# Kernel optimization log

Hardware: AMD Instinct MI355X
Metric: run time of the kernel (lower is better)

## Reference

```python
import jax, jax.numpy as jnp
import numpy as np
import math

B, S, HID, H = 2, 1024, 512, 8
D = HID // H  # 64
EPS = 1e-24


def setup_inputs() -> dict:
    key = jax.random.key(0)
    ks = jax.random.split(key, 12)
    s = 0.02
    return {
        "input_tensor": jax.random.normal(ks[0], (B, S, HID), dtype=jnp.float32),
        "attention_mask": jnp.zeros((B, 1, S, S), dtype=jnp.float32),
        # Linear weights stored as [in, out] (y = x @ W + b)
        "Wq": jax.random.normal(ks[1], (HID, HID), dtype=jnp.float32) * s,
        "bq": jnp.zeros((HID,), dtype=jnp.float32),
        "Wk": jax.random.normal(ks[2], (HID, HID), dtype=jnp.float32) * s,
        "bk": jnp.zeros((HID,), dtype=jnp.float32),
        "Wv": jax.random.normal(ks[3], (HID, HID), dtype=jnp.float32) * s,
        "bv": jnp.zeros((HID,), dtype=jnp.float32),
        # order_affine: Linear(2*D, 1)
        "order_w": jax.random.normal(ks[4], (2 * D,), dtype=jnp.float32) * s,
        "order_b": jnp.zeros((), dtype=jnp.float32),
        # distance_affine: Linear(2*D, 1)
        "dist_w": jax.random.normal(ks[5], (2 * D,), dtype=jnp.float32) * s,
        "dist_b": jnp.zeros((), dtype=jnp.float32),
        "scalar": jax.random.normal(ks[6], (1,), dtype=jnp.float32),
    }


def _heads(x):  # [B,S,HID] -> [B,H,S,D]
    return x.reshape(B, S, H, D).transpose(0, 2, 1, 3)


def reference(input_tensor, attention_mask, Wq, bq, Wk, bk, Wv, bv,
              order_w, order_b, dist_w, dist_b, scalar):
    scale = math.sqrt(D)

    mixed_q = input_tensor @ Wq + bq            # [B,S,HID]
    mixed_k = input_tensor @ Wk + bk
    mixed_v = input_tensor @ Wv + bv

    qh = _heads(mixed_q)                        # [B,H,S,D]
    kh = _heads(mixed_k)
    vh = _heads(mixed_v)

    scores = jnp.einsum('bhid,bhjd->bhij', qh, kh)   # [B,H,S,S]
    origin_scores = scores

    # --- order bias: sigmoid(affine(cat(q_i, k_j))) decomposed (same math,
    # avoids materializing the [B,H,S,S,2D] concat the torch code builds) ---
    q_ord = jnp.einsum('bhid,d->bhi', qh, order_w[:D])    # [B,H,S]
    k_ord = jnp.einsum('bhjd,d->bhj', kh, order_w[D:])
    pr_order = jax.nn.sigmoid(q_ord[..., :, None] + k_ord[..., None, :] + order_b)
    gd_order = jnp.triu(jnp.ones((S, S), dtype=scores.dtype), k=1)  # 1 where j>i
    error_order = (jnp.log(pr_order + EPS) * gd_order
                   + jnp.log(1.0 - pr_order + EPS) * (1.0 - gd_order))

    # --- distance bias ---
    idx = jnp.arange(S)
    gd_distance = jnp.log(jnp.abs(idx[None, :] - idx[:, None]).astype(scores.dtype) + 1.0)
    q_dst = jnp.einsum('bhid,d->bhi', qh, dist_w[:D])
    k_dst = jnp.einsum('bhjd,d->bhj', kh, dist_w[D:])
    pr_distance = q_dst[..., :, None] + k_dst[..., None, :] + dist_b   # [B,H,S,S]
    error_distance = -jnp.square(gd_distance - pr_distance) * jnp.square(scalar[0]) * 0.5

    adj_scores = scores + error_order + error_distance

    def _probs(sc):
        return jax.nn.softmax(sc / scale + attention_mask, axis=-1)

    attention_probs = _probs(adj_scores)
    origin_attention_probs = _probs(origin_scores)

    return (mixed_q, mixed_k, vh, attention_probs, origin_attention_probs)
```

## Files before the change

kernel.cpp:

```cpp
#include <hip/hip_runtime.h>
#include <math.h>

#define Sdim 1024
#define HIDdim 512
#define Hnum 8
#define Ddim 64

typedef __attribute__((ext_vector_type(4))) float f32x4;
typedef __attribute__((ext_vector_type(8))) short short8;
typedef __attribute__((ext_vector_type(4))) unsigned short ushort4v;

static __device__ __forceinline__ unsigned short f2bf(float x) {
    union { float f; unsigned u; } v; v.f = x;
    unsigned r = v.u + 0x7fffu + ((v.u >> 16) & 1u);
    return (unsigned short)(r >> 16);
}

__global__ __launch_bounds__(256) void qkv_gemm(
    const float* __restrict__ X,
    const float* __restrict__ Wq, const float* __restrict__ bq,
    const float* __restrict__ Wk, const float* __restrict__ bk,
    const float* __restrict__ Wv, const float* __restrict__ bv,
    float* __restrict__ outq, float* __restrict__ outk, float* __restrict__ outv)
{
    __shared__ unsigned short Ws[64][72];
    __shared__ unsigned short Xs[64][72];

    const int mb = blockIdx.x;
    const int nb = blockIdx.y;
    const int which = nb >> 3;
    const int n0 = (nb & 7) * 64;
    const float* __restrict__ W    = (which == 0) ? Wq : (which == 1) ? Wk : Wv;
    const float* __restrict__ bias = (which == 0) ? bq : (which == 1) ? bk : bv;

    const int t    = threadIdx.x;
    const int lane = t & 63;
    const int w    = t >> 6;
    const int g    = lane >> 4;
    const int c    = lane & 15;
    const int m0r  = mb * 64;

    f32x4 acc[4];
#pragma unroll
    for (int f = 0; f < 4; ++f) { f32x4 z = {0.f, 0.f, 0.f, 0.f}; acc[f] = z; }

    for (int kt = 0; kt < 512; kt += 64) {
        __syncthreads();
        {
            const int row = t >> 2, kb = (t & 3) * 16;
            const float* __restrict__ src = &X[(size_t)(m0r + row) * HIDdim + kt + kb];
#pragma unroll
            for (int i = 0; i < 4; ++i) {
                const f32x4 v = *(const f32x4*)&src[4 * i];
                ushort4v p;
                p.x = f2bf(v.x); p.y = f2bf(v.y); p.z = f2bf(v.z); p.w = f2bf(v.w);
                *(ushort4v*)&Xs[row][kb + 4 * i] = p;
            }
        }
#pragma unroll
        for (int p = 0; p < 4; ++p) {
            const int kr   = p * 16 + (t >> 4);
            const int nloc = (t & 15) * 4;
            const f32x4 v = *(const f32x4*)&W[(size_t)(kt + kr) * HIDdim + n0 + nloc];
            Ws[nloc + 0][kr] = f2bf(v.x);
            Ws[nloc + 1][kr] = f2bf(v.y);
            Ws[nloc + 2][kr] = f2bf(v.z);
            Ws[nloc + 3][kr] = f2bf(v.w);
        }
        __syncthreads();
        const short8 a0 = *(const short8*)&Ws[w * 16 + c][g * 8];
        const short8 a1 = *(const short8*)&Ws[w * 16 + c][32 + g * 8];
#pragma unroll
        for (int f = 0; f < 4; ++f) {
            const short8 b0 = *(const short8*)&Xs[f * 16 + c][g * 8];
            const short8 b1 = *(const short8*)&Xs[f * 16 + c][32 + g * 8];
            acc[f] = __builtin_amdgcn_mfma_f32_16x16x32_bf16(a0, b0, acc[f], 0, 0, 0);
            acc[f] = __builtin_amdgcn_mfma_f32_16x16x32_bf16(a1, b1, acc[f], 0, 0, 0);
        }
    }

    const int nql = w * 16 + g * 4;
    const f32x4 bb = *(const f32x4*)&bias[n0 + nql];
#pragma unroll
    for (int f = 0; f < 4; ++f) {
        const int m = m0r + f * 16 + c;
        f32x4 v = acc[f] + bb;
        if (which == 2) {
            const int b = m >> 10, s = m & 1023;
            const int h = nb & 7;
            *(f32x4*)&outv[((((size_t)b * Hnum + h) * Sdim) + s) * Ddim + nql] = v;
        } else {
            float* __restrict__ o = (which == 0) ? outq : outk;
            *(f32x4*)&o[(size_t)m * HIDdim + n0 + nql] = v;
        }
    }
}

__global__ __launch_bounds__(512, 4) void attn_kernel(
    const float* __restrict__ mq, const float* __restrict__ mk,
    const float* __restrict__ mask,
    const float* __restrict__ order_w, const float* __restrict__ order_b_p,
    const float* __restrict__ dist_w,  const float* __restrict__ dist_b_p,
    const float* __restrict__ scalar_p,
    float* __restrict__ out_adj, float* __restrict__ out_orig)
{
    __shared__ unsigned short Qs[16][72];
    __shared__ unsigned short Ks[128][72];
    __shared__ float ko_s[Sdim];
    __shared__ float kd_s[Sdim];
    __shared__ float gdl[Sdim];
    __shared__ float qo_s[16], qd_s[16];
    __shared__ float red_s[16][8];

    const int t    = threadIdx.x;
    const int lane = t & 63;
    const int w    = t >> 6;
    const int g    = lane >> 4;
    const int c    = lane & 15;

    const int blk = blockIdx.x;
    const int ib  = blk & 63;
    const int bh  = blk >> 6;
    const int b   = bh >> 3;
    const int h   = bh & 7;
    const int i0  = ib * 16;
    const int i   = i0 + c;

    const float order_b = order_b_p[0];
    const float dist_b  = dist_b_p[0];
    const float sc      = scalar_p[0];
    const float sc2h    = 0.5f * sc * sc;
    const float mscale  = 0.125f;

    const int row8 = t >> 3;
    const int dc8  = (t & 7) * 8;
    const f32x4 owk0 = *(const f32x4*)&order_w[Ddim + dc8];
    const f32x4 owk1 = *(const f32x4*)&order_w[Ddim + dc8 + 4];
    const f32x4 dwk0 = *(const f32x4*)&dist_w[Ddim + dc8];
    const f32x4 dwk1 = *(const f32x4*)&dist_w[Ddim + dc8 + 4];

    if (t < 256) {
        const int drow = t >> 4, dcol = (t & 15) * 4;
        const f32x4 owq = *(const f32x4*)&order_w[dcol];
        const f32x4 dwq = *(const f32x4*)&dist_w[dcol];
        const f32x4 v = *(const f32x4*)&mq[((size_t)b * Sdim + i0 + drow) * HIDdim + h * Ddim + dcol];
        float po = v.x * owq.x + v.y * owq.y + v.z * owq.z + v.w * owq.w;
        float pd = v.x * dwq.x + v.y * dwq.y + v.z * dwq.z + v.w * dwq.w;
#pragma unroll
        for (int o = 1; o < 16; o <<= 1) { po += __shfl_xor(po, o); pd += __shfl_xor(pd, o); }
        if ((t & 15) == 0) { qo_s[drow] = po; qd_s[drow] = pd; }
        ushort4v p;
        p.x = f2bf(v.x); p.y = f2bf(v.y); p.z = f2bf(v.z); p.w = f2bf(v.w);
        *(ushort4v*)&Qs[drow][dcol] = p;
    }
    {
        const int idx = t * 2;
        gdl[idx]     = __logf((float)idx + 1.0f);
        gdl[idx + 1] = __logf((float)idx + 2.0f);
    }
    __syncthreads();

    const short8 qf0 = *(const short8*)&Qs[c][g * 8];
    const short8 qf1 = *(const short8*)&Qs[c][32 + g * 8];

    f32x4 acc[8];
#pragma unroll
    for (int it = 0; it < 8; ++it) { f32x4 z = {0.f, 0.f, 0.f, 0.f}; acc[it] = z; }

#pragma unroll
    for (int it = 0; it < 8; ++it) {
        __syncthreads();
        const int kt0 = it * 128;
#pragma unroll
        for (int sub = 0; sub < 2; ++sub) {
            const int row = sub * 64 + row8;
            const float* __restrict__ src =
                &mk[((size_t)b * Sdim + kt0 + row) * HIDdim + h * Ddim + dc8];
            const f32x4 v0 = *(const f32x4*)&src[0];
            const f32x4 v1 = *(const f32x4*)&src[4];
            float po = v0.x * owk0.x + v0.y * owk0.y + v0.z * owk0.z + v0.w * owk0.w
                     + v1.x * owk1.x + v1.y * owk1.y + v1.z * owk1.z + v1.w * owk1.w;
            float pd = v0.x * dwk0.x + v0.y * dwk0.y + v0.z * dwk0.z + v0.w * dwk0.w
                     + v1.x * dwk1.x + v1.y * dwk1.y + v1.z * dwk1.z + v1.w * dwk1.w;
#pragma unroll
            for (int o = 1; o < 8; o <<= 1) { po += __shfl_xor(po, o); pd += __shfl_xor(pd, o); }
            if ((t & 7) == 0) { ko_s[kt0 + row] = po; kd_s[kt0 + row] = pd; }
            ushort4v p0, p1;
            p0.x = f2bf(v0.x); p0.y = f2bf(v0.y); p0.z = f2bf(v0.z); p0.w = f2bf(v0.w);
            p1.x = f2bf(v1.x); p1.y = f2bf(v1.y); p1.z = f2bf(v1.z); p1.w = f2bf(v1.w);
            *(ushort4v*)&Ks[row][dc8]     = p0;
            *(ushort4v*)&Ks[row][dc8 + 4] = p1;
        }
        __syncthreads();
        const short8 kf0 = *(const short8*)&Ks[w * 16 + c][g * 8];
        const short8 kf1 = *(const short8*)&Ks[w * 16 + c][32 + g * 8];
        acc[it] = __builtin_amdgcn_mfma_f32_16x16x32_bf16(kf0, qf0, acc[it], 0, 0, 0);
        acc[it] = __builtin_amdgcn_mfma_f32_16x16x32_bf16(kf1, qf1, acc[it], 0, 0, 0);
    }

    const size_t obase = (size_t)bh * Sdim * Sdim;
    const float* __restrict__ mrow = &mask[((size_t)b * Sdim + i) * Sdim];

    float s0 = 0.0f;
#pragma unroll
    for (int it = 0; it < 8; ++it) {
        const int j0 = it * 128 + w * 16 + g * 4;
        const f32x4 mk4 = *(const f32x4*)&mrow[j0];
        f32x4 l = acc[it] * mscale + mk4;
        acc[it] = l;
        s0 += __expf(l[0]) + __expf(l[1]) + __expf(l[2]) + __expf(l[3]);
    }
    s0 += __shfl_xor(s0, 16);
    s0 += __shfl_xor(s0, 32);
    if (lane < 16) red_s[lane][w] = s0;
    __syncthreads();
    f32x4 ra = *(const f32x4*)&red_s[c][0];
    f32x4 rb = *(const f32x4*)&red_s[c][4];
    const float inv0 = __builtin_amdgcn_rcpf(ra[0] + ra[1] + ra[2] + ra[3]
                                           + rb[0] + rb[1] + rb[2] + rb[3]);
    {
        float* __restrict__ orow = out_orig + obase + (size_t)i * Sdim;
#pragma unroll
        for (int it = 0; it < 8; ++it) {
            const int j0 = it * 128 + w * 16 + g * 4;
            const f32x4 l = acc[it];
            f32x4 p;
            p[0] = __expf(l[0]) * inv0; p[1] = __expf(l[1]) * inv0;
            p[2] = __expf(l[2]) * inv0; p[3] = __expf(l[3]) * inv0;
            *(f32x4*)&orow[j0] = p;
        }
    }

    const float qo = qo_s[c] + order_b;
    const float qd = qd_s[c] + dist_b;
    float s1 = 0.0f;
#pragma unroll
    for (int it = 0; it < 8; ++it) {
        const int j0 = it * 128 + w * 16 + g * 4;
        const f32x4 ko4 = *(const f32x4*)&ko_s[j0];
        const f32x4 kd4 = *(const f32x4*)&kd_s[j0];
        f32x4 l = acc[it];
#pragma unroll
        for (int r = 0; r < 4; ++r) {
            const int j = j0 + r;
            const float z    = qo + ko4[r];
            const float targ = (j > i) ? -z : z;
            const float pe   = -__logf(1.0f + __expf(targ));
            const int   dl   = (i > j) ? (i - j) : (j - i);
            const float df   = gdl[dl] - (qd + kd4[r]);
            l[r] += (pe - sc2h * df * df) * mscale;
            s1 += __expf(l[r]);
        }
        acc[it] = l;
    }
    __syncthreads();
    s1 += __shfl_xor(s1, 16);
    s1 += __shfl_xor(s1, 32);
    if (lane < 16) red_s[lane][w] = s1;
    __syncthreads();
    ra = *(const f32x4*)&red_s[c][0];
    rb = *(const f32x4*)&red_s[c][4];
    const float inv1 = __builtin_amdgcn_rcpf(ra[0] + ra[1] + ra[2] + ra[3]
                                           + rb[0] + rb[1] + rb[2] + rb[3]);
    {
        float* __restrict__ arow = out_adj + obase + (size_t)i * Sdim;
#pragma unroll
        for (int it = 0; it < 8; ++it) {
            const int j0 = it * 128 + w * 16 + g * 4;
            const f32x4 l = acc[it];
            f32x4 p;
            p[0] = __expf(l[0]) * inv1; p[1] = __expf(l[1]) * inv1;
            p[2] = __expf(l[2]) * inv1; p[3] = __expf(l[3]) * inv1;
            *(f32x4*)&arow[j0] = p;
        }
    }
}

extern "C" void kernel_launch(void* const* d_in, const int* in_sizes, int n_in,
                              void* d_out, int out_size, void* d_ws, size_t ws_size,
                              hipStream_t stream) {
    const float* X    = (const float*)d_in[0];
    const float* mask = (const float*)d_in[1];
    const float* Wq   = (const float*)d_in[2];
    const float* bq   = (const float*)d_in[3];
    const float* Wk   = (const float*)d_in[4];
    const float* bk   = (const float*)d_in[5];
    const float* Wv   = (const float*)d_in[6];
    const float* bv   = (const float*)d_in[7];
    const float* ow   = (const float*)d_in[8];
    const float* ob   = (const float*)d_in[9];
    const float* dw   = (const float*)d_in[10];
    const float* db   = (const float*)d_in[11];
    const float* sc   = (const float*)d_in[12];

    float* out     = (float*)d_out;
    float* outq    = out;
    float* outk    = out + 1048576;
    float* outv    = out + 2097152;
    float* outadj  = out + 3145728;
    float* outorig = out + 19922944;

    qkv_gemm<<<dim3(32, 24), 256, 0, stream>>>(X, Wq, bq, Wk, bk, Wv, bv,
                                               outq, outk, outv);
    attn_kernel<<<dim3(1024), 512, 0, stream>>>(outq, outk, mask,
                                                ow, ob, dw, db, sc,
                                                outadj, outorig);
}
```

Measured before the change: 82.28 us.

## Precompute bf16 Q/K and bias projections in a separate prep kernel

```diff
diff --git a/kernel.cpp b/kernel.cpp
--- a/kernel.cpp
+++ b/kernel.cpp
@@ -96,20 +96,73 @@
     }
 }
 
+__global__ __launch_bounds__(256) void prep_kernel(
+    const float* __restrict__ mq, const float* __restrict__ mk,
+    const float* __restrict__ order_w, const float* __restrict__ dist_w,
+    unsigned short* __restrict__ qbf, unsigned short* __restrict__ kbf,
+    float* __restrict__ qog, float* __restrict__ qdg,
+    float* __restrict__ kog, float* __restrict__ kdg)
+{
+    const int tg  = blockIdx.x * 256 + threadIdx.x;
+    const int row = tg >> 3;
+    const int dc8 = (tg & 7) * 8;
+    const int bh  = row >> 10, s = row & 1023;
+    const int b   = bh >> 3,   h = bh & 7;
+    const size_t src = ((size_t)b * Sdim + s) * HIDdim + h * Ddim + dc8;
+
+    const f32x4 ow0 = *(const f32x4*)&order_w[dc8];
+    const f32x4 ow1 = *(const f32x4*)&order_w[dc8 + 4];
+    const f32x4 dw0 = *(const f32x4*)&dist_w[dc8];
+    const f32x4 dw1 = *(const f32x4*)&dist_w[dc8 + 4];
+    const f32x4 owk0 = *(const f32x4*)&order_w[Ddim + dc8];
+    const f32x4 owk1 = *(const f32x4*)&order_w[Ddim + dc8 + 4];
+    const f32x4 dwk0 = *(const f32x4*)&dist_w[Ddim + dc8];
+    const f32x4 dwk1 = *(const f32x4*)&dist_w[Ddim + dc8 + 4];
+
+    {
+        const f32x4 v0 = *(const f32x4*)&mq[src];
+        const f32x4 v1 = *(const f32x4*)&mq[src + 4];
+        float po = v0.x * ow0.x + v0.y * ow0.y + v0.z * ow0.z + v0.w * ow0.w
+                 + v1.x * ow1.x + v1.y * ow1.y + v1.z * ow1.z + v1.w * ow1.w;
+        float pd = v0.x * dw0.x + v0.y * dw0.y + v0.z * dw0.z + v0.w * dw0.w
+                 + v1.x * dw1.x + v1.y * dw1.y + v1.z * dw1.z + v1.w * dw1.w;
+#pragma unroll
+        for (int o = 1; o < 8; o <<= 1) { po += __shfl_xor(po, o); pd += __shfl_xor(pd, o); }
+        if ((tg & 7) == 0) { qog[row] = po; qdg[row] = pd; }
+        ushort4v p0, p1;
+        p0.x = f2bf(v0.x); p0.y = f2bf(v0.y); p0.z = f2bf(v0.z); p0.w = f2bf(v0.w);
+        p1.x = f2bf(v1.x); p1.y = f2bf(v1.y); p1.z = f2bf(v1.z); p1.w = f2bf(v1.w);
+        *(ushort4v*)&qbf[(size_t)row * Ddim + dc8]     = p0;
+        *(ushort4v*)&qbf[(size_t)row * Ddim + dc8 + 4] = p1;
+    }
+    {
+        const f32x4 v0 = *(const f32x4*)&mk[src];
+        const f32x4 v1 = *(const f32x4*)&mk[src + 4];
+        float po = v0.x * owk0.x + v0.y * owk0.y + v0.z * owk0.z + v0.w * owk0.w
+                 + v1.x * owk1.x + v1.y * owk1.y + v1.z * owk1.z + v1.w * owk1.w;
+        float pd = v0.x * dwk0.x + v0.y * dwk0.y + v0.z * dwk0.z + v0.w * dwk0.w
+                 + v1.x * dwk1.x + v1.y * dwk1.y + v1.z * dwk1.z + v1.w * dwk1.w;
+#pragma unroll
+        for (int o = 1; o < 8; o <<= 1) { po += __shfl_xor(po, o); pd += __shfl_xor(pd, o); }
+        if ((tg & 7) == 0) { kog[row] = po; kdg[row] = pd; }
+        ushort4v p0, p1;
+        p0.x = f2bf(v0.x); p0.y = f2bf(v0.y); p0.z = f2bf(v0.z); p0.w = f2bf(v0.w);
+        p1.x = f2bf(v1.x); p1.y = f2bf(v1.y); p1.z = f2bf(v1.z); p1.w = f2bf(v1.w);
+        *(ushort4v*)&kbf[(size_t)row * Ddim + dc8]     = p0;
+        *(ushort4v*)&kbf[(size_t)row * Ddim + dc8 + 4] = p1;
+    }
+}
+
 __global__ __launch_bounds__(512, 4) void attn_kernel(
-    const float* __restrict__ mq, const float* __restrict__ mk,
+    const unsigned short* __restrict__ qbf, const unsigned short* __restrict__ kbf,
+    const float* __restrict__ qog, const float* __restrict__ qdg,
+    const float* __restrict__ kog, const float* __restrict__ kdg,
     const float* __restrict__ mask,
-    const float* __restrict__ order_w, const float* __restrict__ order_b_p,
-    const float* __restrict__ dist_w,  const float* __restrict__ dist_b_p,
+    const float* __restrict__ order_b_p, const float* __restrict__ dist_b_p,
     const float* __restrict__ scalar_p,
     float* __restrict__ out_adj, float* __restrict__ out_orig)
 {
-    __shared__ unsigned short Qs[16][72];
-    __shared__ unsigned short Ks[128][72];
-    __shared__ float ko_s[Sdim];
-    __shared__ float kd_s[Sdim];
     __shared__ float gdl[Sdim];
-    __shared__ float qo_s[16], qd_s[16];
     __shared__ float red_s[16][8];
 
     const int t    = threadIdx.x;
@@ -122,7 +175,6 @@
     const int ib  = blk & 63;
     const int bh  = blk >> 6;
     const int b   = bh >> 3;
-    const int h   = bh & 7;
     const int i0  = ib * 16;
     const int i   = i0 + c;
 
@@ -132,27 +184,6 @@
     const float sc2h    = 0.5f * sc * sc;
     const float mscale  = 0.125f;
 
-    const int row8 = t >> 3;
-    const int dc8  = (t & 7) * 8;
-    const f32x4 owk0 = *(const f32x4*)&order_w[Ddim + dc8];
-    const f32x4 owk1 = *(const f32x4*)&order_w[Ddim + dc8 + 4];
-    const f32x4 dwk0 = *(const f32x4*)&dist_w[Ddim + dc8];
-    const f32x4 dwk1 = *(const f32x4*)&dist_w[Ddim + dc8 + 4];
-
-    if (t < 256) {
-        const int drow = t >> 4, dcol = (t & 15) * 4;
-        const f32x4 owq = *(const f32x4*)&order_w[dcol];
-        const f32x4 dwq = *(const f32x4*)&dist_w[dcol];
-        const f32x4 v = *(const f32x4*)&mq[((size_t)b * Sdim + i0 + drow) * HIDdim + h * Ddim + dcol];
-        float po = v.x * owq.x + v.y * owq.y + v.z * owq.z + v.w * owq.w;
-        float pd = v.x * dwq.x + v.y * dwq.y + v.z * dwq.z + v.w * dwq.w;
-#pragma unroll
-        for (int o = 1; o < 16; o <<= 1) { po += __shfl_xor(po, o); pd += __shfl_xor(pd, o); }
-        if ((t & 15) == 0) { qo_s[drow] = po; qd_s[drow] = pd; }
-        ushort4v p;
-        p.x = f2bf(v.x); p.y = f2bf(v.y); p.z = f2bf(v.z); p.w = f2bf(v.w);
-        *(ushort4v*)&Qs[drow][dcol] = p;
-    }
     {
         const int idx = t * 2;
         gdl[idx]     = __logf((float)idx + 1.0f);
@@ -160,8 +191,10 @@
     }
     __syncthreads();
 
-    const short8 qf0 = *(const short8*)&Qs[c][g * 8];
-    const short8 qf1 = *(const short8*)&Qs[c][32 + g * 8];
+    const size_t hbase = (size_t)bh * Sdim;
+    const size_t qrow = (hbase + i) * Ddim;
+    const short8 qf0 = *(const short8*)&qbf[qrow + g * 8];
+    const short8 qf1 = *(const short8*)&qbf[qrow + 32 + g * 8];
 
     f32x4 acc[8];
 #pragma unroll
@@ -169,31 +202,9 @@
 
 #pragma unroll
     for (int it = 0; it < 8; ++it) {
-        __syncthreads();
-        const int kt0 = it * 128;
-#pragma unroll
-        for (int sub = 0; sub < 2; ++sub) {
-            const int row = sub * 64 + row8;
-            const float* __restrict__ src =
-                &mk[((size_t)b * Sdim + kt0 + row) * HIDdim + h * Ddim + dc8];
-            const f32x4 v0 = *(const f32x4*)&src[0];
-            const f32x4 v1 = *(const f32x4*)&src[4];
-            float po = v0.x * owk0.x + v0.y * owk0.y + v0.z * owk0.z + v0.w * owk0.w
-                     + v1.x * owk1.x + v1.y * owk1.y + v1.z * owk1.z + v1.w * owk1.w;
-            float pd = v0.x * dwk0.x + v0.y * dwk0.y + v0.z * dwk0.z + v0.w * dwk0.w
-                     + v1.x * dwk1.x + v1.y * dwk1.y + v1.z * dwk1.z + v1.w * dwk1.w;
-#pragma unroll
-            for (int o = 1; o < 8; o <<= 1) { po += __shfl_xor(po, o); pd += __shfl_xor(pd, o); }
-            if ((t & 7) == 0) { ko_s[kt0 + row] = po; kd_s[kt0 + row] = pd; }
-            ushort4v p0, p1;
-            p0.x = f2bf(v0.x); p0.y = f2bf(v0.y); p0.z = f2bf(v0.z); p0.w = f2bf(v0.w);
-            p1.x = f2bf(v1.x); p1.y = f2bf(v1.y); p1.z = f2bf(v1.z); p1.w = f2bf(v1.w);
-            *(ushort4v*)&Ks[row][dc8]     = p0;
-            *(ushort4v*)&Ks[row][dc8 + 4] = p1;
-        }
-        __syncthreads();
-        const short8 kf0 = *(const short8*)&Ks[w * 16 + c][g * 8];
-        const short8 kf1 = *(const short8*)&Ks[w * 16 + c][32 + g * 8];
+        const size_t kr = (hbase + it * 128 + w * 16 + c) * Ddim;
+        const short8 kf0 = *(const short8*)&kbf[kr + g * 8];
+        const short8 kf1 = *(const short8*)&kbf[kr + 32 + g * 8];
         acc[it] = __builtin_amdgcn_mfma_f32_16x16x32_bf16(kf0, qf0, acc[it], 0, 0, 0);
         acc[it] = __builtin_amdgcn_mfma_f32_16x16x32_bf16(kf1, qf1, acc[it], 0, 0, 0);
     }
@@ -231,14 +242,14 @@
         }
     }
 
-    const float qo = qo_s[c] + order_b;
-    const float qd = qd_s[c] + dist_b;
+    const float qo = qog[hbase + i] + order_b;
+    const float qd = qdg[hbase + i] + dist_b;
     float s1 = 0.0f;
 #pragma unroll
     for (int it = 0; it < 8; ++it) {
         const int j0 = it * 128 + w * 16 + g * 4;
-        const f32x4 ko4 = *(const f32x4*)&ko_s[j0];
-        const f32x4 kd4 = *(const f32x4*)&kd_s[j0];
+        const f32x4 ko4 = *(const f32x4*)&kog[hbase + j0];
+        const f32x4 kd4 = *(const f32x4*)&kdg[hbase + j0];
         f32x4 l = acc[it];
 #pragma unroll
         for (int r = 0; r < 4; ++r) {
@@ -300,9 +311,18 @@
     float* outadj  = out + 3145728;
     float* outorig = out + 19922944;
 
+    unsigned short* qbf = (unsigned short*)d_ws;
+    unsigned short* kbf = qbf + 16384 * 64;
+    float* qog = (float*)(kbf + 16384 * 64);
+    float* qdg = qog + 16384;
+    float* kog = qdg + 16384;
+    float* kdg = kog + 16384;
+
     qkv_gemm<<<dim3(32, 24), 256, 0, stream>>>(X, Wq, bq, Wk, bk, Wv, bv,
                                                outq, outk, outv);
-    attn_kernel<<<dim3(1024), 512, 0, stream>>>(outq, outk, mask,
-                                                ow, ob, dw, db, sc,
+    prep_kernel<<<dim3(512), 256, 0, stream>>>(outq, outk, ow, dw,
+                                               qbf, kbf, qog, qdg, kog, kdg);
+    attn_kernel<<<dim3(1024), 512, 0, stream>>>(qbf, kbf, qog, qdg, kog, kdg,
+                                                mask, ob, db, sc,
                                                 outadj, outorig);
 }
```

New measurement: 83.03 us. Within noise of the previous version (+0.9%).
